# Optimization experiments

Measured on AMD Instinct MI355X. Metric: run time of the kernel, lower is better.

## Reference

```python
import jax, jax.numpy as jnp
import numpy as np

# dims: batch, input, output, state, heads, shifts, slot size, num addresses
B, IN, OUT, ST, H, NSHIFT, M, N = 256, 256, 256, 512, 4, 3, 64, 1024
READ = H * M
PPH = NSHIFT + 1 + M + M + M + 1 + 1  # per-head params: s, gamma, erase, add, k, beta, g
UPD = H * PPH
D = IN + ST + READ  # controller input width
_IDX = np.cumsum([0, NSHIFT, 1, M, M, M, 1, 1]).tolist()


def setup_inputs() -> dict:
    key = jax.random.key(0)
    ks = jax.random.split(key, 8)
    sc = 0.05
    tm_input = jax.random.normal(ks[0], (B, IN), jnp.float32)
    tm_state = jax.random.uniform(ks[1], (B, ST), jnp.float32)
    wt = jax.nn.softmax(jax.random.normal(ks[2], (B, H, N), jnp.float32), axis=-1)
    mem = jax.random.normal(ks[3], (B, N, M), jnp.float32) * 0.1
    return {
        'tm_input': tm_input, 'tm_state': tm_state, 'wt': wt, 'mem': mem,
        'W_i2w': jax.random.normal(ks[4], (H, ST + IN), jnp.float32) * sc,
        'b_i2w': jnp.zeros((H,), jnp.float32),
        'W_i2s': jax.random.normal(ks[5], (ST, D), jnp.float32) * sc,
        'b_i2s': jnp.zeros((ST,), jnp.float32),
        'W_i2o': jax.random.normal(ks[6], (OUT, D), jnp.float32) * sc,
        'b_i2o': jnp.zeros((OUT,), jnp.float32),
        'W_i2u': jax.random.normal(ks[7], (UPD, D), jnp.float32) * sc,
        'b_i2u': jnp.zeros((UPD,), jnp.float32),
    }


def _ntm_cell(tm_input, tm_state, wt, mem,
              W_i2w, b_i2w, W_i2s, b_i2s, W_i2o, b_i2o, W_i2u, b_i2u):
    # --- gated reset of attention toward address 0 ---
    combined = jnp.concatenate([tm_state, tm_input], axis=-1)        # [B, ST+IN]
    f = jax.nn.sigmoid(combined @ W_i2w.T + b_i2w)[..., None]        # [B, H, 1]
    wt0 = jnp.zeros_like(wt).at[:, :, 0].set(1.0)
    wt = f * wt0 + (1.0 - f) * wt                                    # [B, H, N]

    # --- interface read ---
    read = jnp.einsum('bhn,bnm->bhm', wt, mem).reshape(wt.shape[0], READ)

    # --- controller ---
    c = jnp.concatenate([tm_input, tm_state, read], axis=-1)         # [B, D]
    tm_state_new = jax.nn.sigmoid(c @ W_i2s.T + b_i2s)
    tm_output = jax.nn.sigmoid(c @ W_i2o.T + b_i2o)
    ud = (c @ W_i2u.T + b_i2u).reshape(-1, H, PPH)                   # [B, H, PPH]

    # --- split + activate interface parameters ---
    s_sh  = jax.nn.softmax(jax.nn.softplus(ud[..., _IDX[0]:_IDX[1]]), axis=-1)  # shift
    gamma = 1.0 + jax.nn.softplus(ud[..., _IDX[1]:_IDX[2]])                      # sharpening
    erase = jax.nn.sigmoid(ud[..., _IDX[2]:_IDX[3]])
    add   = jnp.tanh(ud[..., _IDX[3]:_IDX[4]])
    k     = jnp.tanh(ud[..., _IDX[4]:_IDX[5]])
    beta  = jax.nn.softplus(ud[..., _IDX[5]:_IDX[6]])
    g     = jax.nn.sigmoid(ud[..., _IDX[6]:_IDX[7]])

    # --- write: multiplicative erase over heads, then additive write ---
    keep = jnp.prod(1.0 - wt[..., None] * erase[:, :, None, :], axis=1)  # [B, N, M]
    mem = mem * keep + jnp.einsum('bhn,bhm->bnm', wt, add)

    # --- content addressing (cosine similarity) + gated interpolation ---
    kn = k / (jnp.linalg.norm(k, axis=-1, keepdims=True) + 1e-8)
    mn = mem / (jnp.linalg.norm(mem, axis=-1, keepdims=True) + 1e-8)
    sim = jnp.einsum('bhm,bnm->bhn', kn, mn)
    wt = g * jax.nn.softmax(beta * sim, axis=-1) + (1.0 - g) * wt

    # --- circular convolution with the shift kernel ---
    zone = NSHIFT // 2
    wt = sum(s_sh[..., j + zone, None] * jnp.roll(wt, j, axis=-1)
             for j in range(-zone, zone + 1))

    # --- sharpening + L1 renormalization ---
    wt = (wt + 1e-12) ** gamma
    wt = wt / jnp.sum(wt, axis=-1, keepdims=True)

    return tm_output, tm_state_new, wt, mem


def reference(tm_input, tm_state, wt, mem,
              W_i2w, b_i2w, W_i2s, b_i2s, W_i2o, b_i2o, W_i2u, b_i2u):
    return _ntm_cell(tm_input, tm_state, wt, mem,
                     W_i2w, b_i2w, W_i2s, b_i2s, W_i2o, b_i2o, W_i2u, b_i2u)
```

## Files before the change

kernel.cpp:

```cpp
#include <hip/hip_runtime.h>
#include <math.h>

#define B_    256
#define IN_   256
#define OUT_  256
#define ST_   512
#define H_    4
#define M_    64
#define N_    1024
#define D_    1024
#define PPH_  198
#define UPD_  792
#define NTOT  1560
#define CP_   1600
#define KS_   4
#define RCH_  4
#define WCONV_BLKS 780

typedef unsigned short ushort_;
typedef unsigned int uint_;

typedef __attribute__((ext_vector_type(8))) short bf16x8;
typedef __attribute__((ext_vector_type(4))) float f32x4;

__device__ __forceinline__ float sigmoidf_(float x){ return 1.f/(1.f+__expf(-x)); }
__device__ __forceinline__ float softplusf_(float x){
    float ax = fabsf(x);
    return fmaxf(x, 0.f) + log1pf(__expf(-ax));
}
__device__ __forceinline__ ushort_ f2bf(float f){
    uint_ u = __float_as_uint(f);
    u += 0x7fffu + ((u >> 16) & 1u);
    return (ushort_)(u >> 16);
}

__global__ __launch_bounds__(256) void k_front(
    const float* __restrict__ tm_input, const float* __restrict__ tm_state,
    const float* __restrict__ wt, const float* __restrict__ mem,
    const float* __restrict__ W_i2w, const float* __restrict__ b_i2w,
    const float* __restrict__ W_i2s, const float* __restrict__ W_i2o,
    const float* __restrict__ W_i2u, ushort_* __restrict__ Wb,
    float* __restrict__ wt_g, ushort_* __restrict__ cB,
    float* __restrict__ Pr)
{
    const int bid = blockIdx.x;
    if (bid >= B_*RCH_) {
        const int idx = ((bid - B_*RCH_)*256 + threadIdx.x) * 8;
        const float* src;
        if (idx < 512*1024)      src = W_i2s + idx;
        else if (idx < 768*1024) src = W_i2o + (idx - 512*1024);
        else                     src = W_i2u + (idx - 768*1024);
        float4 v0 = *(const float4*)src;
        float4 v1 = *(const float4*)(src + 4);
        union { ushort_ u[8]; uint4 q; } r;
        r.u[0]=f2bf(v0.x); r.u[1]=f2bf(v0.y); r.u[2]=f2bf(v0.z); r.u[3]=f2bf(v0.w);
        r.u[4]=f2bf(v1.x); r.u[5]=f2bf(v1.y); r.u[6]=f2bf(v1.z); r.u[7]=f2bf(v1.w);
        *(uint4*)(Wb + idx) = r.q;
        return;
    }

    __shared__ float wt_sl[256*H_];
    __shared__ float part[4][H_][M_];
    __shared__ float f_s[H_];
    const int b = bid >> 2, chunk = bid & 3, tid = threadIdx.x;
    const int wave = tid >> 6, lane = tid & 63;
    const float* st  = tm_state + (size_t)b*ST_;
    const float* inp = tm_input + (size_t)b*IN_;

    {
        float pa = 0.f;
        const float* Wrow = W_i2w + wave*(ST_+IN_);
        #pragma unroll
        for (int k = 0; k < 12; ++k) {
            int i = lane + 64*k;
            float v = (i < ST_) ? st[i] : inp[i - ST_];
            pa += v * Wrow[i];
        }
        #pragma unroll
        for (int m = 32; m; m >>= 1) pa += __shfl_xor(pa, m, 64);
        if (lane == 0) f_s[wave] = sigmoidf_(pa + b_i2w[wave]);
    }
    if (chunk == 0) {
        #pragma unroll
        for (int i = 0; i < 3; ++i) {
            int j = tid + 256*i;
            cB[(size_t)b*D_ + j] = f2bf(j < IN_ ? inp[j] : st[j - IN_]);
        }
    }
    __syncthreads();

    const int nbase = chunk * 256;
    #pragma unroll
    for (int i = 0; i < 4; ++i) {
        int idx = tid + 256*i;
        int h = idx & 3, nl = idx >> 2;
        int n = nbase + nl;
        float f = f_s[h];
        float v = (1.f - f) * wt[((size_t)b*H_ + h)*N_ + n];
        if (n == 0) v += f;
        wt_sl[idx] = v;
        wt_g[((size_t)b*H_ + h)*N_ + n] = v;
    }
    __syncthreads();

    {
        const int m4 = lane & 15, ro = lane >> 4;
        const float4* mp = (const float4*)(mem + ((size_t)b*N_ + nbase)*M_);
        float4 a0 = make_float4(0.f,0.f,0.f,0.f), a1 = a0, a2 = a0, a3 = a0;
        #pragma unroll
        for (int r = 0; r < 16; ++r) {
            const int nl = wave*64 + r*4 + ro;
            const float4 mv = mp[nl*16 + m4];
            const float4 wv = *(const float4*)&wt_sl[nl*4];
            a0.x += wv.x*mv.x; a0.y += wv.x*mv.y; a0.z += wv.x*mv.z; a0.w += wv.x*mv.w;
            a1.x += wv.y*mv.x; a1.y += wv.y*mv.y; a1.z += wv.y*mv.z; a1.w += wv.y*mv.w;
            a2.x += wv.z*mv.x; a2.y += wv.z*mv.y; a2.z += wv.z*mv.z; a2.w += wv.z*mv.w;
            a3.x += wv.w*mv.x; a3.y += wv.w*mv.y; a3.z += wv.w*mv.z; a3.w += wv.w*mv.w;
        }
        #pragma unroll
        for (int msk = 16; msk <= 32; msk <<= 1) {
            a0.x += __shfl_xor(a0.x, msk, 64); a0.y += __shfl_xor(a0.y, msk, 64);
            a0.z += __shfl_xor(a0.z, msk, 64); a0.w += __shfl_xor(a0.w, msk, 64);
            a1.x += __shfl_xor(a1.x, msk, 64); a1.y += __shfl_xor(a1.y, msk, 64);
            a1.z += __shfl_xor(a1.z, msk, 64); a1.w += __shfl_xor(a1.w, msk, 64);
            a2.x += __shfl_xor(a2.x, msk, 64); a2.y += __shfl_xor(a2.y, msk, 64);
            a2.z += __shfl_xor(a2.z, msk, 64); a2.w += __shfl_xor(a2.w, msk, 64);
            a3.x += __shfl_xor(a3.x, msk, 64); a3.y += __shfl_xor(a3.y, msk, 64);
            a3.z += __shfl_xor(a3.z, msk, 64); a3.w += __shfl_xor(a3.w, msk, 64);
        }
        if (ro == 0) {
            *(float4*)&part[wave][0][m4*4] = a0;
            *(float4*)&part[wave][1][m4*4] = a1;
            *(float4*)&part[wave][2][m4*4] = a2;
            *(float4*)&part[wave][3][m4*4] = a3;
        }
    }
    __syncthreads();
    {
        const int h = tid >> 6, m = tid & 63;
        float r = part[0][h][m] + part[1][h][m] + part[2][h][m] + part[3][h][m];
        Pr[((size_t)(b*RCH_ + chunk))*256 + tid] = r;
    }
}

__global__ __launch_bounds__(256) void k_read_merge(
    const float* __restrict__ Pr, ushort_* __restrict__ cB)
{
    const int b = blockIdx.x, tid = threadIdx.x;
    float r = 0.f;
    #pragma unroll
    for (int c = 0; c < RCH_; ++c)
        r += Pr[((size_t)(b*RCH_ + c))*256 + tid];
    cB[(size_t)b*D_ + IN_ + ST_ + tid] = f2bf(r);
}

__global__ __launch_bounds__(256) void k_ctrl_gemm_mfma(
    const ushort_* __restrict__ cB, const ushort_* __restrict__ Wb,
    float* __restrict__ P)
{
    const int tid = threadIdx.x;
    const int w = tid >> 6, lane = tid & 63;
    const int wr = w >> 1, wc = w & 1;
    const int b0 = blockIdx.y * 64 + wr * 32;
    const int o0 = blockIdx.x * 64 + wc * 32;
    const int kb = blockIdx.z * (D_ / KS_);
    const int lrow = lane & 15, lk = (lane >> 4) * 8;

    const bf16x8* a0p = (const bf16x8*)(cB + (size_t)(b0 + lrow)*D_ + kb + lk);
    const bf16x8* a1p = (const bf16x8*)(cB + (size_t)(b0 + 16 + lrow)*D_ + kb + lk);
    const int oc0 = min(o0 + lrow, NTOT-1);
    const int oc1 = min(o0 + 16 + lrow, NTOT-1);
    const bf16x8* b0p = (const bf16x8*)(Wb + (size_t)oc0*D_ + kb + lk);
    const bf16x8* b1p = (const bf16x8*)(Wb + (size_t)oc1*D_ + kb + lk);

    f32x4 acc00 = {0.f,0.f,0.f,0.f}, acc01 = acc00, acc10 = acc00, acc11 = acc00;
    #pragma unroll
    for (int ks = 0; ks < (D_/KS_)/32; ++ks) {
        bf16x8 av0 = a0p[ks*4];
        bf16x8 av1 = a1p[ks*4];
        bf16x8 bv0 = b0p[ks*4];
        bf16x8 bv1 = b1p[ks*4];
        acc00 = __builtin_amdgcn_mfma_f32_16x16x32_bf16(av0, bv0, acc00, 0, 0, 0);
        acc01 = __builtin_amdgcn_mfma_f32_16x16x32_bf16(av0, bv1, acc01, 0, 0, 0);
        acc10 = __builtin_amdgcn_mfma_f32_16x16x32_bf16(av1, bv0, acc10, 0, 0, 0);
        acc11 = __builtin_amdgcn_mfma_f32_16x16x32_bf16(av1, bv1, acc11, 0, 0, 0);
    }

    float* Pp = P + (size_t)blockIdx.z * (B_*CP_);
    const int rsub = (lane >> 4) * 4;
    #pragma unroll
    for (int mi = 0; mi < 2; ++mi) {
        #pragma unroll
        for (int ni = 0; ni < 2; ++ni) {
            f32x4 v = (mi == 0) ? (ni == 0 ? acc00 : acc01)
                                : (ni == 0 ? acc10 : acc11);
            const int o = o0 + ni*16 + lrow;
            const int rbase = b0 + mi*16 + rsub;
            #pragma unroll
            for (int r = 0; r < 4; ++r)
                Pp[(size_t)(rbase + r)*CP_ + o] = v[r];
        }
    }
}

__global__ __launch_bounds__(256) void k_memsim(
    const float* __restrict__ mem, const float* __restrict__ wt_g,
    const float* __restrict__ P, const float* __restrict__ b_i2u,
    float* __restrict__ mem_out, float* __restrict__ sim)
{
    __shared__ float es[H_*M_], as[H_*M_], ks[H_*M_];
    const int tid = threadIdx.x;
    const int b = blockIdx.x >> 4;
    const int chunk = blockIdx.x & 15;
    const int wave = tid >> 6, lane = tid & 63;

    {
        const int m = lane;
        const size_t pb = (size_t)b*CP_ + 768 + wave*PPH_;
        #define ULOAD(j) (P[pb+(j)] + P[(size_t)B_*CP_+pb+(j)] \
                        + P[2*(size_t)B_*CP_+pb+(j)] + P[3*(size_t)B_*CP_+pb+(j)] \
                        + b_i2u[wave*PPH_+(j)])
        float ev = sigmoidf_(ULOAD(4 + m));
        float av = tanhf(ULOAD(68 + m));
        float kv = tanhf(ULOAD(132 + m));
        #undef ULOAD
        float ss = kv*kv;
        #pragma unroll
        for (int msk = 32; msk; msk >>= 1) ss += __shfl_xor(ss, msk, 64);
        es[tid] = ev;
        as[tid] = av;
        ks[tid] = kv / (sqrtf(ss) + 1e-8f);
    }
    __syncthreads();

    const int q = lane & 3, rloc = lane >> 2;
    const int n = chunk*64 + wave*16 + rloc;

    const float w0 = wt_g[((size_t)b*H_ + 0)*N_ + n];
    const float w1 = wt_g[((size_t)b*H_ + 1)*N_ + n];
    const float w2 = wt_g[((size_t)b*H_ + 2)*N_ + n];
    const float w3 = wt_g[((size_t)b*H_ + 3)*N_ + n];

    const float4* mp = (const float4*)(mem     + ((size_t)b*N_ + n)*M_ + q*16);
    float4*       op = (float4*)      (mem_out + ((size_t)b*N_ + n)*M_ + q*16);

    float nrm = 0.f, p0 = 0.f, p1 = 0.f, p2 = 0.f, p3 = 0.f;
    #pragma unroll
    for (int jj = 0; jj < 4; ++jj) {
        const int c4 = q*16 + jj*4;
        const float4 o  = mp[jj];
        const float4 e0 = *(const float4*)&es[      c4];
        const float4 e1 = *(const float4*)&es[ 64 + c4];
        const float4 e2 = *(const float4*)&es[128 + c4];
        const float4 e3 = *(const float4*)&es[192 + c4];
        const float4 a0 = *(const float4*)&as[      c4];
        const float4 a1 = *(const float4*)&as[ 64 + c4];
        const float4 a2 = *(const float4*)&as[128 + c4];
        const float4 a3 = *(const float4*)&as[192 + c4];
        const float4 k0 = *(const float4*)&ks[      c4];
        const float4 k1 = *(const float4*)&ks[ 64 + c4];
        const float4 k2 = *(const float4*)&ks[128 + c4];
        const float4 k3 = *(const float4*)&ks[192 + c4];

        float4 nm;
        nm.x = o.x*((1.f-w0*e0.x)*(1.f-w1*e1.x)*(1.f-w2*e2.x)*(1.f-w3*e3.x))
             + (w0*a0.x + w1*a1.x + w2*a2.x + w3*a3.x);
        nm.y = o.y*((1.f-w0*e0.y)*(1.f-w1*e1.y)*(1.f-w2*e2.y)*(1.f-w3*e3.y))
             + (w0*a0.y + w1*a1.y + w2*a2.y + w3*a3.y);
        nm.z = o.z*((1.f-w0*e0.z)*(1.f-w1*e1.z)*(1.f-w2*e2.z)*(1.f-w3*e3.z))
             + (w0*a0.z + w1*a1.z + w2*a2.z + w3*a3.z);
        nm.w = o.w*((1.f-w0*e0.w)*(1.f-w1*e1.w)*(1.f-w2*e2.w)*(1.f-w3*e3.w))
             + (w0*a0.w + w1*a1.w + w2*a2.w + w3*a3.w);
        op[jj] = nm;

        nrm += nm.x*nm.x + nm.y*nm.y + nm.z*nm.z + nm.w*nm.w;
        p0 += k0.x*nm.x + k0.y*nm.y + k0.z*nm.z + k0.w*nm.w;
        p1 += k1.x*nm.x + k1.y*nm.y + k1.z*nm.z + k1.w*nm.w;
        p2 += k2.x*nm.x + k2.y*nm.y + k2.z*nm.z + k2.w*nm.w;
        p3 += k3.x*nm.x + k3.y*nm.y + k3.z*nm.z + k3.w*nm.w;
    }
    #pragma unroll
    for (int msk = 1; msk <= 2; msk <<= 1) {
        nrm += __shfl_xor(nrm, msk, 64);
        p0  += __shfl_xor(p0,  msk, 64);
        p1  += __shfl_xor(p1,  msk, 64);
        p2  += __shfl_xor(p2,  msk, 64);
        p3  += __shfl_xor(p3,  msk, 64);
    }
    const float inv = 1.f/(sqrtf(nrm) + 1e-8f);
    const float pv = (q == 0) ? p0 : (q == 1) ? p1 : (q == 2) ? p2 : p3;
    sim[((size_t)b*H_ + q)*N_ + n] = pv*inv;
}

__global__ __launch_bounds__(256) void k_wt_final(
    const float* __restrict__ sim, const float* __restrict__ wt_g,
    const float* __restrict__ P,
    const float* __restrict__ b_i2s, const float* __restrict__ b_i2o,
    const float* __restrict__ b_i2u,
    float* __restrict__ out, float* __restrict__ wt_out)
{
    __shared__ float wc[N_];
    __shared__ float red[8];
    const int bh = blockIdx.x, tid = threadIdx.x, wave = tid >> 6, lane = tid & 63;
    const int b = bh >> 2, h = bh & 3;

    if (tid < 192) {
        const int o = h*192 + tid;
        const size_t base = (size_t)b*CP_ + o;
        float v = P[base] + P[(size_t)B_*CP_ + base]
                + P[2*(size_t)B_*CP_ + base] + P[3*(size_t)B_*CP_ + base];
        if (o < ST_)
            out[(size_t)B_*OUT_ + (size_t)b*ST_ + o] = sigmoidf_(v + b_i2s[o]);
        else
            out[(size_t)b*OUT_ + (o - ST_)] = sigmoidf_(v + b_i2o[o - ST_]);
    }

    const size_t pb = (size_t)b*CP_ + 768 + h*PPH_;
    #define ULOAD(j) (P[pb+(j)] + P[(size_t)B_*CP_+pb+(j)] \
                    + P[2*(size_t)B_*CP_+pb+(j)] + P[3*(size_t)B_*CP_+pb+(j)] \
                    + b_i2u[h*PPH_+(j)])
    const float sp0 = softplusf_(ULOAD(0));
    const float sp1 = softplusf_(ULOAD(1));
    const float sp2 = softplusf_(ULOAD(2));
    const float gamma = 1.f + softplusf_(ULOAD(3));
    const float beta  = softplusf_(ULOAD(196));
    const float g     = sigmoidf_(ULOAD(197));
    #undef ULOAD
    const float mx3 = fmaxf(sp0, fmaxf(sp1, sp2));
    const float ee0 = __expf(sp0-mx3), ee1 = __expf(sp1-mx3), ee2 = __expf(sp2-mx3);
    const float inv3 = 1.f/(ee0+ee1+ee2);
    const float s0 = ee0*inv3, s1 = ee1*inv3, s2 = ee2*inv3;

    const float* simp = sim + (size_t)bh*N_;
    const float* wgp  = wt_g + (size_t)bh*N_;

    float x[4];
    float mx = -1e30f;
    #pragma unroll
    for (int i = 0; i < 4; ++i) { x[i] = beta*simp[tid + 256*i]; mx = fmaxf(mx, x[i]); }
    #pragma unroll
    for (int msk = 32; msk; msk >>= 1) mx = fmaxf(mx, __shfl_xor(mx, msk, 64));
    if (lane == 0) red[wave] = mx;
    __syncthreads();
    mx = fmaxf(fmaxf(red[0], red[1]), fmaxf(red[2], red[3]));

    float e[4]; float sum = 0.f;
    #pragma unroll
    for (int i = 0; i < 4; ++i) { e[i] = __expf(x[i] - mx); sum += e[i]; }
    #pragma unroll
    for (int msk = 32; msk; msk >>= 1) sum += __shfl_xor(sum, msk, 64);
    if (lane == 0) red[4 + wave] = sum;
    __syncthreads();
    sum = red[4] + red[5] + red[6] + red[7];
    const float inv = 1.f/sum;

    #pragma unroll
    for (int i = 0; i < 4; ++i) {
        int n = tid + 256*i;
        wc[n] = g*e[i]*inv + (1.f - g)*wgp[n];
    }
    __syncthreads();

    float y[4]; float ysum = 0.f;
    #pragma unroll
    for (int i = 0; i < 4; ++i) {
        int n = tid + 256*i;
        float v = s0*wc[(n+1) & (N_-1)] + s1*wc[n] + s2*wc[(n-1) & (N_-1)];
        y[i] = __powf(v + 1e-12f, gamma);
        ysum += y[i];
    }
    #pragma unroll
    for (int msk = 32; msk; msk >>= 1) ysum += __shfl_xor(ysum, msk, 64);
    __syncthreads();
    if (lane == 0) red[wave] = ysum;
    __syncthreads();
    ysum = red[0] + red[1] + red[2] + red[3];
    const float yinv = 1.f/ysum;
    #pragma unroll
    for (int i = 0; i < 4; ++i)
        wt_out[(size_t)bh*N_ + tid + 256*i] = y[i]*yinv;
}

extern "C" void kernel_launch(void* const* d_in, const int* in_sizes, int n_in,
                              void* d_out, int out_size, void* d_ws, size_t ws_size,
                              hipStream_t stream)
{
    const float* tm_input = (const float*)d_in[0];
    const float* tm_state = (const float*)d_in[1];
    const float* wt       = (const float*)d_in[2];
    const float* mem      = (const float*)d_in[3];
    const float* W_i2w    = (const float*)d_in[4];
    const float* b_i2w    = (const float*)d_in[5];
    const float* W_i2s    = (const float*)d_in[6];
    const float* b_i2s    = (const float*)d_in[7];
    const float* W_i2o    = (const float*)d_in[8];
    const float* b_i2o    = (const float*)d_in[9];
    const float* W_i2u    = (const float*)d_in[10];
    const float* b_i2u    = (const float*)d_in[11];

    float* out = (float*)d_out;
    float* ws  = (float*)d_ws;

    float*   wt_g  = ws;
    ushort_* cB    = (ushort_*)(ws + 1048576);
    ushort_* Wb    = (ushort_*)(ws + 1179648);
    float*   P     = ws + 1978368;
    float*   Pr    = ws + 3616768;

    float* out_wt  = out + 196608;
    float* out_mem = out + 1245184;

    hipLaunchKernelGGL(k_front, dim3(B_*RCH_ + WCONV_BLKS), dim3(256), 0, stream,
                       tm_input, tm_state, wt, mem, W_i2w, b_i2w,
                       W_i2s, W_i2o, W_i2u, Wb, wt_g, cB, Pr);
    hipLaunchKernelGGL(k_read_merge, dim3(B_), dim3(256), 0, stream,
                       Pr, cB);
    hipLaunchKernelGGL(k_ctrl_gemm_mfma, dim3(25, 4, KS_), dim3(256), 0, stream,
                       cB, Wb, P);
    hipLaunchKernelGGL(k_memsim, dim3(B_*16), dim3(256), 0, stream,
                       mem, wt_g, P, b_i2u, out_mem, out_wt);
    hipLaunchKernelGGL(k_wt_final, dim3(B_*H_), dim3(256), 0, stream,
                       out_wt, wt_g, P, b_i2s, b_i2o, b_i2u, out, out_wt);
}
```

Measured before the change: 78.14 us.

## Fuse memory update/similarity and weight finalization into one per-batch kernel

Merges the memory write/cosine-similarity kernel and the attention-weight finalization kernel into a single kernel with one 1024-thread block per batch element. Similarities and the old weights stay in shared memory, which removes the global round trip for sim, one launch, and the separate output sigmoid pass. In exchange the grid shrinks from 4096 small blocks to 256 large ones. This may reduce latency hiding on the bandwidth-bound memory stream, and the per-head softmax/shift/sharpen loop now runs serially with many block-wide barriers.

```diff
diff --git a/kernel.cpp b/kernel.cpp
--- a/kernel.cpp
+++ b/kernel.cpp
@@ -203,18 +203,23 @@
     }
 }
 
-__global__ __launch_bounds__(256) void k_memsim(
+__global__ __launch_bounds__(1024) void k_memsim_wt(
     const float* __restrict__ mem, const float* __restrict__ wt_g,
-    const float* __restrict__ P, const float* __restrict__ b_i2u,
-    float* __restrict__ mem_out, float* __restrict__ sim)
+    const float* __restrict__ P,
+    const float* __restrict__ b_i2s, const float* __restrict__ b_i2o,
+    const float* __restrict__ b_i2u,
+    float* __restrict__ out, float* __restrict__ mem_out,
+    float* __restrict__ wt_out)
 {
     __shared__ float es[H_*M_], as[H_*M_], ks[H_*M_];
-    const int tid = threadIdx.x;
-    const int b = blockIdx.x >> 4;
-    const int chunk = blockIdx.x & 15;
+    __shared__ float wgs[H_][N_];
+    __shared__ float sims[H_][N_];
+    __shared__ float wc[N_];
+    __shared__ float red[32];
+    const int b = blockIdx.x, tid = threadIdx.x;
     const int wave = tid >> 6, lane = tid & 63;
 
-    {
+    if (tid < 256) {
         const int m = lane;
         const size_t pb = (size_t)b*CP_ + 768 + wave*PPH_;
         #define ULOAD(j) (P[pb+(j)] + P[(size_t)B_*CP_+pb+(j)] \
@@ -230,82 +235,8 @@
         es[tid] = ev;
         as[tid] = av;
         ks[tid] = kv / (sqrtf(ss) + 1e-8f);
-    }
-    __syncthreads();
-
-    const int q = lane & 3, rloc = lane >> 2;
-    const int n = chunk*64 + wave*16 + rloc;
-
-    const float w0 = wt_g[((size_t)b*H_ + 0)*N_ + n];
-    const float w1 = wt_g[((size_t)b*H_ + 1)*N_ + n];
-    const float w2 = wt_g[((size_t)b*H_ + 2)*N_ + n];
-    const float w3 = wt_g[((size_t)b*H_ + 3)*N_ + n];
-
-    const float4* mp = (const float4*)(mem     + ((size_t)b*N_ + n)*M_ + q*16);
-    float4*       op = (float4*)      (mem_out + ((size_t)b*N_ + n)*M_ + q*16);
-
-    float nrm = 0.f, p0 = 0.f, p1 = 0.f, p2 = 0.f, p3 = 0.f;
-    #pragma unroll
-    for (int jj = 0; jj < 4; ++jj) {
-        const int c4 = q*16 + jj*4;
-        const float4 o  = mp[jj];
-        const float4 e0 = *(const float4*)&es[      c4];
-        const float4 e1 = *(const float4*)&es[ 64 + c4];
-        const float4 e2 = *(const float4*)&es[128 + c4];
-        const float4 e3 = *(const float4*)&es[192 + c4];
-        const float4 a0 = *(const float4*)&as[      c4];
-        const float4 a1 = *(const float4*)&as[ 64 + c4];
-        const float4 a2 = *(const float4*)&as[128 + c4];
-        const float4 a3 = *(const float4*)&as[192 + c4];
-        const float4 k0 = *(const float4*)&ks[      c4];
-        const float4 k1 = *(const float4*)&ks[ 64 + c4];
-        const float4 k2 = *(const float4*)&ks[128 + c4];
-        const float4 k3 = *(const float4*)&ks[192 + c4];
-
-        float4 nm;
-        nm.x = o.x*((1.f-w0*e0.x)*(1.f-w1*e1.x)*(1.f-w2*e2.x)*(1.f-w3*e3.x))
-             + (w0*a0.x + w1*a1.x + w2*a2.x + w3*a3.x);
-        nm.y = o.y*((1.f-w0*e0.y)*(1.f-w1*e1.y)*(1.f-w2*e2.y)*(1.f-w3*e3.y))
-             + (w0*a0.y + w1*a1.y + w2*a2.y + w3*a3.y);
-        nm.z = o.z*((1.f-w0*e0.z)*(1.f-w1*e1.z)*(1.f-w2*e2.z)*(1.f-w3*e3.z))
-             + (w0*a0.z + w1*a1.z + w2*a2.z + w3*a3.z);
-        nm.w = o.w*((1.f-w0*e0.w)*(1.f-w1*e1.w)*(1.f-w2*e2.w)*(1.f-w3*e3.w))
-             + (w0*a0.w + w1*a1.w + w2*a2.w + w3*a3.w);
-        op[jj] = nm;
-
-        nrm += nm.x*nm.x + nm.y*nm.y + nm.z*nm.z + nm.w*nm.w;
-        p0 += k0.x*nm.x + k0.y*nm.y + k0.z*nm.z + k0.w*nm.w;
-        p1 += k1.x*nm.x + k1.y*nm.y + k1.z*nm.z + k1.w*nm.w;
-        p2 += k2.x*nm.x + k2.y*nm.y + k2.z*nm.z + k2.w*nm.w;
-        p3 += k3.x*nm.x + k3.y*nm.y + k3.z*nm.z + k3.w*nm.w;
-    }
-    #pragma unroll
-    for (int msk = 1; msk <= 2; msk <<= 1) {
-        nrm += __shfl_xor(nrm, msk, 64);
-        p0  += __shfl_xor(p0,  msk, 64);
-        p1  += __shfl_xor(p1,  msk, 64);
-        p2  += __shfl_xor(p2,  msk, 64);
-        p3  += __shfl_xor(p3,  msk, 64);
-    }
-    const float inv = 1.f/(sqrtf(nrm) + 1e-8f);
-    const float pv = (q == 0) ? p0 : (q == 1) ? p1 : (q == 2) ? p2 : p3;
-    sim[((size_t)b*H_ + q)*N_ + n] = pv*inv;
-}
-
-__global__ __launch_bounds__(256) void k_wt_final(
-    const float* __restrict__ sim, const float* __restrict__ wt_g,
-    const float* __restrict__ P,
-    const float* __restrict__ b_i2s, const float* __restrict__ b_i2o,
-    const float* __restrict__ b_i2u,
-    float* __restrict__ out, float* __restrict__ wt_out)
-{
-    __shared__ float wc[N_];
-    __shared__ float red[8];
-    const int bh = blockIdx.x, tid = threadIdx.x, wave = tid >> 6, lane = tid & 63;
-    const int b = bh >> 2, h = bh & 3;
-
-    if (tid < 192) {
-        const int o = h*192 + tid;
+    } else {
+        const int o = tid - 256;
         const size_t base = (size_t)b*CP_ + o;
         float v = P[base] + P[(size_t)B_*CP_ + base]
                 + P[2*(size_t)B_*CP_ + base] + P[3*(size_t)B_*CP_ + base];
@@ -314,71 +245,129 @@
         else
             out[(size_t)b*OUT_ + (o - ST_)] = sigmoidf_(v + b_i2o[o - ST_]);
     }
-
-    const size_t pb = (size_t)b*CP_ + 768 + h*PPH_;
-    #define ULOAD(j) (P[pb+(j)] + P[(size_t)B_*CP_+pb+(j)] \
-                    + P[2*(size_t)B_*CP_+pb+(j)] + P[3*(size_t)B_*CP_+pb+(j)] \
-                    + b_i2u[h*PPH_+(j)])
-    const float sp0 = softplusf_(ULOAD(0));
-    const float sp1 = softplusf_(ULOAD(1));
-    const float sp2 = softplusf_(ULOAD(2));
-    const float gamma = 1.f + softplusf_(ULOAD(3));
-    const float beta  = softplusf_(ULOAD(196));
-    const float g     = sigmoidf_(ULOAD(197));
-    #undef ULOAD
-    const float mx3 = fmaxf(sp0, fmaxf(sp1, sp2));
-    const float ee0 = __expf(sp0-mx3), ee1 = __expf(sp1-mx3), ee2 = __expf(sp2-mx3);
-    const float inv3 = 1.f/(ee0+ee1+ee2);
-    const float s0 = ee0*inv3, s1 = ee1*inv3, s2 = ee2*inv3;
-
-    const float* simp = sim + (size_t)bh*N_;
-    const float* wgp  = wt_g + (size_t)bh*N_;
-
-    float x[4];
-    float mx = -1e30f;
-    #pragma unroll
-    for (int i = 0; i < 4; ++i) { x[i] = beta*simp[tid + 256*i]; mx = fmaxf(mx, x[i]); }
-    #pragma unroll
-    for (int msk = 32; msk; msk >>= 1) mx = fmaxf(mx, __shfl_xor(mx, msk, 64));
-    if (lane == 0) red[wave] = mx;
+    #pragma unroll
+    for (int i = 0; i < 4; ++i) {
+        int idx = tid + 1024*i;
+        wgs[idx >> 10][idx & (N_-1)] = wt_g[(size_t)b*H_*N_ + idx];
+    }
     __syncthreads();
-    mx = fmaxf(fmaxf(red[0], red[1]), fmaxf(red[2], red[3]));
-
-    float e[4]; float sum = 0.f;
-    #pragma unroll
-    for (int i = 0; i < 4; ++i) { e[i] = __expf(x[i] - mx); sum += e[i]; }
-    #pragma unroll
-    for (int msk = 32; msk; msk >>= 1) sum += __shfl_xor(sum, msk, 64);
-    if (lane == 0) red[4 + wave] = sum;
+
+    const int q = lane & 3, rloc = lane >> 2;
+    #pragma unroll
+    for (int pass = 0; pass < 4; ++pass) {
+        const int n = pass*256 + wave*16 + rloc;
+
+        const float w0 = wgs[0][n];
+        const float w1 = wgs[1][n];
+        const float w2 = wgs[2][n];
+        const float w3 = wgs[3][n];
+
+        const float4* mp = (const float4*)(mem     + ((size_t)b*N_ + n)*M_ + q*16);
+        float4*       op = (float4*)      (mem_out + ((size_t)b*N_ + n)*M_ + q*16);
+
+        float nrm = 0.f, p0 = 0.f, p1 = 0.f, p2 = 0.f, p3 = 0.f;
+        #pragma unroll
+        for (int jj = 0; jj < 4; ++jj) {
+            const int c4 = q*16 + jj*4;
+            const float4 o  = mp[jj];
+            const float4 e0 = *(const float4*)&es[      c4];
+            const float4 e1 = *(const float4*)&es[ 64 + c4];
+            const float4 e2 = *(const float4*)&es[128 + c4];
+            const float4 e3 = *(const float4*)&es[192 + c4];
+            const float4 a0 = *(const float4*)&as[      c4];
+            const float4 a1 = *(const float4*)&as[ 64 + c4];
+            const float4 a2 = *(const float4*)&as[128 + c4];
+            const float4 a3 = *(const float4*)&as[192 + c4];
+            const float4 k0 = *(const float4*)&ks[      c4];
+            const float4 k1 = *(const float4*)&ks[ 64 + c4];
+            const float4 k2 = *(const float4*)&ks[128 + c4];
+            const float4 k3 = *(const float4*)&ks[192 + c4];
+
+            float4 nm;
+            nm.x = o.x*((1.f-w0*e0.x)*(1.f-w1*e1.x)*(1.f-w2*e2.x)*(1.f-w3*e3.x))
+                 + (w0*a0.x + w1*a1.x + w2*a2.x + w3*a3.x);
+            nm.y = o.y*((1.f-w0*e0.y)*(1.f-w1*e1.y)*(1.f-w2*e2.y)*(1.f-w3*e3.y))
+                 + (w0*a0.y + w1*a1.y + w2*a2.y + w3*a3.y);
+            nm.z = o.z*((1.f-w0*e0.z)*(1.f-w1*e1.z)*(1.f-w2*e2.z)*(1.f-w3*e3.z))
+                 + (w0*a0.z + w1*a1.z + w2*a2.z + w3*a3.z);
+            nm.w = o.w*((1.f-w0*e0.w)*(1.f-w1*e1.w)*(1.f-w2*e2.w)*(1.f-w3*e3.w))
+                 + (w0*a0.w + w1*a1.w + w2*a2.w + w3*a3.w);
+            op[jj] = nm;
+
+            nrm += nm.x*nm.x + nm.y*nm.y + nm.z*nm.z + nm.w*nm.w;
+            p0 += k0.x*nm.x + k0.y*nm.y + k0.z*nm.z + k0.w*nm.w;
+            p1 += k1.x*nm.x + k1.y*nm.y + k1.z*nm.z + k1.w*nm.w;
+            p2 += k2.x*nm.x + k2.y*nm.y + k2.z*nm.z + k2.w*nm.w;
+            p3 += k3.x*nm.x + k3.y*nm.y + k3.z*nm.z + k3.w*nm.w;
+        }
+        #pragma unroll
+        for (int msk = 1; msk <= 2; msk <<= 1) {
+            nrm += __shfl_xor(nrm, msk, 64);
+            p0  += __shfl_xor(p0,  msk, 64);
+            p1  += __shfl_xor(p1,  msk, 64);
+            p2  += __shfl_xor(p2,  msk, 64);
+            p3  += __shfl_xor(p3,  msk, 64);
+        }
+        const float inv = 1.f/(sqrtf(nrm) + 1e-8f);
+        const float pv = (q == 0) ? p0 : (q == 1) ? p1 : (q == 2) ? p2 : p3;
+        sims[q][n] = pv*inv;
+    }
     __syncthreads();
-    sum = red[4] + red[5] + red[6] + red[7];
-    const float inv = 1.f/sum;
-
-    #pragma unroll
-    for (int i = 0; i < 4; ++i) {
-        int n = tid + 256*i;
-        wc[n] = g*e[i]*inv + (1.f - g)*wgp[n];
-    }
-    __syncthreads();
-
-    float y[4]; float ysum = 0.f;
-    #pragma unroll
-    for (int i = 0; i < 4; ++i) {
-        int n = tid + 256*i;
-        float v = s0*wc[(n+1) & (N_-1)] + s1*wc[n] + s2*wc[(n-1) & (N_-1)];
-        y[i] = __powf(v + 1e-12f, gamma);
-        ysum += y[i];
-    }
-    #pragma unroll
-    for (int msk = 32; msk; msk >>= 1) ysum += __shfl_xor(ysum, msk, 64);
-    __syncthreads();
-    if (lane == 0) red[wave] = ysum;
-    __syncthreads();
-    ysum = red[0] + red[1] + red[2] + red[3];
-    const float yinv = 1.f/ysum;
-    #pragma unroll
-    for (int i = 0; i < 4; ++i)
-        wt_out[(size_t)bh*N_ + tid + 256*i] = y[i]*yinv;
+
+    for (int h = 0; h < H_; ++h) {
+        const size_t pb = (size_t)b*CP_ + 768 + h*PPH_;
+        #define ULOAD(j) (P[pb+(j)] + P[(size_t)B_*CP_+pb+(j)] \
+                        + P[2*(size_t)B_*CP_+pb+(j)] + P[3*(size_t)B_*CP_+pb+(j)] \
+                        + b_i2u[h*PPH_+(j)])
+        const float sp0 = softplusf_(ULOAD(0));
+        const float sp1 = softplusf_(ULOAD(1));
+        const float sp2 = softplusf_(ULOAD(2));
+        const float gamma = 1.f + softplusf_(ULOAD(3));
+        const float beta  = softplusf_(ULOAD(196));
+        const float g     = sigmoidf_(ULOAD(197));
+        #undef ULOAD
+        const float mx3 = fmaxf(sp0, fmaxf(sp1, sp2));
+        const float ee0 = __expf(sp0-mx3), ee1 = __expf(sp1-mx3), ee2 = __expf(sp2-mx3);
+        const float inv3 = 1.f/(ee0+ee1+ee2);
+        const float s0 = ee0*inv3, s1 = ee1*inv3, s2 = ee2*inv3;
+
+        float x = beta*sims[h][tid];
+        float mx = x;
+        #pragma unroll
+        for (int msk = 32; msk; msk >>= 1) mx = fmaxf(mx, __shfl_xor(mx, msk, 64));
+        if (lane == 0) red[wave] = mx;
+        __syncthreads();
+        mx = red[0];
+        #pragma unroll
+        for (int i = 1; i < 16; ++i) mx = fmaxf(mx, red[i]);
+
+        float e = __expf(x - mx);
+        float sum = e;
+        #pragma unroll
+        for (int msk = 32; msk; msk >>= 1) sum += __shfl_xor(sum, msk, 64);
+        if (lane == 0) red[16 + wave] = sum;
+        __syncthreads();
+        sum = red[16];
+        #pragma unroll
+        for (int i = 1; i < 16; ++i) sum += red[16 + i];
+        const float invs = 1.f/sum;
+
+        wc[tid] = g*e*invs + (1.f - g)*wgs[h][tid];
+        __syncthreads();
+
+        float v = s0*wc[(tid+1) & (N_-1)] + s1*wc[tid] + s2*wc[(tid-1) & (N_-1)];
+        float y = __powf(v + 1e-12f, gamma);
+        float ysum = y;
+        #pragma unroll
+        for (int msk = 32; msk; msk >>= 1) ysum += __shfl_xor(ysum, msk, 64);
+        if (lane == 0) red[wave] = ysum;
+        __syncthreads();
+        ysum = red[0];
+        #pragma unroll
+        for (int i = 1; i < 16; ++i) ysum += red[i];
+        wt_out[((size_t)b*H_ + h)*N_ + tid] = y/ysum;
+        __syncthreads();
+    }
 }
 
 extern "C" void kernel_launch(void* const* d_in, const int* in_sizes, int n_in,
@@ -417,8 +406,6 @@
                        Pr, cB);
     hipLaunchKernelGGL(k_ctrl_gemm_mfma, dim3(25, 4, KS_), dim3(256), 0, stream,
                        cB, Wb, P);
-    hipLaunchKernelGGL(k_memsim, dim3(B_*16), dim3(256), 0, stream,
-                       mem, wt_g, P, b_i2u, out_mem, out_wt);
-    hipLaunchKernelGGL(k_wt_final, dim3(B_*H_), dim3(256), 0, stream,
-                       out_wt, wt_g, P, b_i2s, b_i2o, b_i2u, out, out_wt);
-}
+    hipLaunchKernelGGL(k_memsim_wt, dim3(B_), dim3(1024), 0, stream,
+                       mem, wt_g, P, b_i2s, b_i2o, b_i2u, out, out_mem, out_wt);
+}
```

New measurement: 92.92 us. 1.19x slower.
